# Kernel optimization log

Hardware: AMD Instinct MI355X
Metric: run time of the kernel (lower is better)

## Reference

```python
import jax, jax.numpy as jnp
import numpy as np

D = 512       # d_model
M = 64        # working memory_dim
SE = 32       # episodic slots
SS = 64       # semantic slots
H = 4         # episodic heads
B, L = 2, 1024
BOT = max(D // 4, 32)  # controller bottleneck = 128


def _layernorm(x, g, b, eps=1e-5):
    mu = jnp.mean(x, axis=-1, keepdims=True)
    var = jnp.var(x, axis=-1, keepdims=True)
    return (x - mu) * jax.lax.rsqrt(var + eps) * g + b


def setup_inputs() -> dict:
    key = jax.random.key(0)
    ks = jax.random.split(key, 24)
    r = lambda i, shape, s=0.02: jax.random.normal(ks[i], shape, dtype=jnp.float32) * s
    return {
        "x": jax.random.normal(ks[0], (B, L, D), dtype=jnp.float32),
        # WorkingMemory (weights stored as (in, out))
        "Wq": r(1, (D, M)), "Wk": r(2, (D, M)), "Wv": r(3, (D, D)),
        "Wf": r(4, (D, M)), "bf": jnp.zeros((M,), jnp.float32),
        "Wo": r(5, (D, D)),
        "ln_g": jnp.ones((D,), jnp.float32), "ln_b": jnp.zeros((D,), jnp.float32),
        # EpisodicMemory
        "eslots": r(6, (1, SE, D)),
        "Eq": r(7, (D, D)), "Ek": r(8, (D, D)), "Ev": r(9, (D, D)), "Eo": r(10, (D, D)),
        # SemanticMemory
        "know": r(11, (1, SS, D)),
        "Sin": r(12, (D, D)),
        "Sg_w": r(13, (D, D)), "Sg_b": jnp.zeros((D,), jnp.float32),
        "So": r(14, (D, D)),
        # MemoryController
        "C1w": r(15, (D, BOT)), "C1b": jnp.zeros((BOT,), jnp.float32),
        "C2w": r(16, (BOT, 3)), "C2b": jnp.zeros((3,), jnp.float32),
    }


def _forward(x, Wq, Wk, Wv, Wf, bf, Wo, ln_g, ln_b,
             eslots, Eq, Ek, Ev, Eo,
             know, Sin, Sg_w, Sg_b, So,
             C1w, C1b, C2w, C2b):
    b, l, d = x.shape
    # ---- WorkingMemory (parallel gated linear attention) ----
    scale = M ** -0.5
    q = (jax.nn.elu(x @ Wq) + 1.0) * scale          # (B,L,M)
    k = jax.nn.elu(x @ Wk) + 1.0                    # (B,L,M)
    v = x @ Wv                                      # (B,L,D)
    forget = jax.nn.sigmoid(x @ Wf + bf)            # (B,L,M)
    log_f_cum = jnp.clip(jnp.cumsum(jnp.log(jnp.clip(forget, 1e-6, None)), axis=1), -20.0, 20.0)
    exp_neg = jnp.exp(-log_f_cum)
    exp_pos = jnp.exp(log_f_cum)
    kv = k[..., :, None] * v[..., None, :]          # (B,L,M,D) outer product
    cum_kv = jnp.cumsum(exp_neg[..., None] * kv, axis=1)
    Mstate = exp_pos[..., None] * cum_kv            # (B,L,M,D)
    z = exp_pos * jnp.cumsum(exp_neg * k, axis=1)   # (B,L,M)
    num = jnp.einsum('blm,blmd->bld', q, Mstate)
    den = jnp.einsum('blm,blm->bl', q, z)[..., None] + 1e-6
    w_out = _layernorm(num / den, ln_g, ln_b) @ Wo  # (B,L,D)

    # ---- EpisodicMemory (cross-attn to learned slots) ----
    hd = D // H
    mem = jnp.broadcast_to(eslots, (b, SE, D))
    qh = (x @ Eq).reshape(b, l, H, hd)
    kh = (mem @ Ek).reshape(b, SE, H, hd)
    vh = (mem @ Ev).reshape(b, SE, H, hd)
    scores = jnp.einsum('blhe,bshe->bhls', qh, kh) / jnp.sqrt(jnp.float32(hd))
    attn = jax.nn.softmax(scores, axis=-1)
    e_out = jnp.einsum('bhls,bshe->blhe', attn, vh).reshape(b, l, D) @ Eo

    # ---- SemanticMemory (single-head attn to knowledge, gated residual) ----
    kb = jnp.broadcast_to(know, (b, SS, D))
    qs = x @ Sin                                    # (B,L,D)
    s_scores = jnp.einsum('bld,bsd->bls', qs, kb) / jnp.sqrt(jnp.float32(D))
    s_attn = jax.nn.softmax(s_scores, axis=-1)
    retrieved = jnp.einsum('bls,bsd->bld', s_attn, kb)
    gate = jax.nn.sigmoid(x @ Sg_w + Sg_b)
    s_out = (gate * retrieved + (1.0 - gate) * x) @ So

    # ---- Controller fusion ----
    wts = jax.nn.softmax(jax.nn.silu(x @ C1w + C1b) @ C2w + C2b, axis=-1)  # (B,L,3)
    fused = (wts[..., 0:1] * w_out + wts[..., 1:2] * e_out + wts[..., 2:3] * s_out)
    return fused


def reference(x, Wq, Wk, Wv, Wf, bf, Wo, ln_g, ln_b,
              eslots, Eq, Ek, Ev, Eo,
              know, Sin, Sg_w, Sg_b, So,
              C1w, C1b, C2w, C2b):
    return _forward(x, Wq, Wk, Wv, Wf, bf, Wo, ln_g, ln_b,
                    eslots, Eq, Ek, Ev, Eo,
                    know, Sin, Sg_w, Sg_b, So,
                    C1w, C1b, C2w, C2b)
```

## Files before the change

kernel.cpp:

```cpp
#include <hip/hip_runtime.h>
#include <cstdint>

typedef unsigned int uint;
typedef unsigned short ushort;
typedef __attribute__((ext_vector_type(8))) short bf16x8;
typedef __attribute__((ext_vector_type(4))) float f32x4;

__device__ __forceinline__ ushort f2b(float f) {
  union { float f; uint u; } v; v.f = f;
  uint u = v.u;
  uint r = (u + 0x7FFFu + ((u >> 16) & 1u)) >> 16;
  return (ushort)r;
}
__device__ __forceinline__ float b2f(ushort h) {
  union { uint u; float f; } v; v.u = ((uint)h) << 16; return v.f;
}

__global__ __launch_bounds__(256) void k_prepA(
    const float* __restrict__ know, const float* __restrict__ eslots,
    const float* __restrict__ Ek, const float* __restrict__ Ev, const float* __restrict__ Sin,
    ushort* __restrict__ Wcat, float* __restrict__ kh, float* __restrict__ vh)
{
  int bid = blockIdx.x;
  int tid = threadIdx.x;
  int lane = tid & 63, wv = tid >> 6;

  if (bid < 256) {
    int k = bid * 2 + (wv >> 1);
    int s0 = (wv & 1) * 32;
    const float* sp = Sin + (size_t)k * 512 + lane * 8;
    float4 s1 = *(const float4*)&sp[0];
    float4 s2 = *(const float4*)&sp[4];
    #pragma unroll 4
    for (int si = 0; si < 32; ++si) {
      int s = s0 + si;
      const float* kp = know + (size_t)s * 512 + lane * 8;
      float4 k1 = *(const float4*)&kp[0];
      float4 k2 = *(const float4*)&kp[4];
      float part = s1.x * k1.x + s1.y * k1.y + s1.z * k1.z + s1.w * k1.w
                 + s2.x * k2.x + s2.y * k2.y + s2.z * k2.z + s2.w * k2.w;
      #pragma unroll
      for (int o = 32; o; o >>= 1) part += __shfl_xor(part, o);
      if (lane == 0) Wcat[(640 + s) * 512 + k] = f2b(part * 0.04419417382415922f);
    }
    return;
  }
  {
    int t = (bid - 256) * 256 + tid;
    int isv = (t >= 16384);
    int o = t & 16383; int s = o >> 9, j = o & 511;
    const float* W = isv ? Ev : Ek;
    const float* es = eslots + (size_t)s * 512;
    float a0 = 0.f, a1 = 0.f, a2 = 0.f, a3 = 0.f;
    #pragma unroll 8
    for (int d = 0; d < 512; d += 4) {
      a0 += es[d + 0] * W[(size_t)(d + 0) * 512 + j];
      a1 += es[d + 1] * W[(size_t)(d + 1) * 512 + j];
      a2 += es[d + 2] * W[(size_t)(d + 2) * 512 + j];
      a3 += es[d + 3] * W[(size_t)(d + 3) * 512 + j];
    }
    float acc = (a0 + a1) + (a2 + a3);
    (isv ? vh : kh)[(size_t)s * 512 + j] = acc;
  }
}

__global__ __launch_bounds__(256) void k_prepB(
    const float* __restrict__ x, const float* __restrict__ Wv, const float* __restrict__ Sg,
    const float* __restrict__ C1w, const float* __restrict__ Wq, const float* __restrict__ Wk,
    const float* __restrict__ Wf, const float* __restrict__ Wo, const float* __restrict__ So,
    const float* __restrict__ Eq, const float* __restrict__ Eo, const float* __restrict__ know,
    const float* __restrict__ kh, const float* __restrict__ vh,
    ushort* __restrict__ X16, ushort* __restrict__ Wcat, ushort* __restrict__ Wfin,
    ushort* __restrict__ know16)
{
  __shared__ __align__(16) float pool[4160];
  int bid = blockIdx.x;
  int tid = threadIdx.x;
  int lane = tid & 63, wv = tid >> 6;

  if (bid < 256) {
    int gw = bid * 4 + wv;
    #pragma unroll
    for (int pp = 0; pp < 2; ++pp) {
      int pair = gw * 2 + pp;
      int k = pair >> 2, h = pair & 3;
      const float* ep = Eq + (size_t)k * 512 + h * 128 + lane * 2;
      float e0 = ep[0], e1 = ep[1];
      #pragma unroll 4
      for (int s = 0; s < 32; ++s) {
        const float* kp = kh + (size_t)s * 512 + h * 128 + lane * 2;
        float part = e0 * kp[0] + e1 * kp[1];
        #pragma unroll
        for (int o = 32; o; o >>= 1) part += __shfl_xor(part, o);
        if (lane == 0) Wcat[(512 + h * 32 + s) * 512 + k] = f2b(part * 0.08838834764831845f);
      }
    }
    return;
  }
  if (bid < 512) {
    int o = (bid - 256) * 256 + tid;
    int hs = o >> 9, j = o & 511;
    int h = hs >> 5, s = hs & 31;
    const float* vhp = vh + (size_t)s * 512 + h * 128;
    float acc = 0.f;
    #pragma unroll 16
    for (int e = 0; e < 128; ++e) acc += vhp[e] * Eo[(size_t)(h * 128 + e) * 512 + j];
    Wfin[(size_t)j * 1152 + 1024 + hs] = f2b(acc);
    return;
  }
  if (bid < 808) {
    #define Tm(a,b) pool[(a) * 65 + (b)]
    int tt = bid - 512;
    const float* src; ushort* dst; int sld, dld, Nt, drow, dcol;
    if (tt < 64)       {           src = Wv;  dst = Wcat; sld = 512; dld = 512;  Nt = 8; drow = 0;    dcol = 0;   }
    else if (tt < 128) { tt -= 64; src = Sg;  dst = Wcat; sld = 512; dld = 512;  Nt = 8; drow = 704;  dcol = 0;   }
    else if (tt < 144) { tt -= 128; src = C1w; dst = Wcat; sld = 128; dld = 512; Nt = 2; drow = 1216; dcol = 0;   }
    else if (tt < 152) { tt -= 144; src = Wq;  dst = Wcat; sld = 64;  dld = 512; Nt = 1; drow = 1344; dcol = 0;   }
    else if (tt < 160) { tt -= 152; src = Wk;  dst = Wcat; sld = 64;  dld = 512; Nt = 1; drow = 1408; dcol = 0;   }
    else if (tt < 168) { tt -= 160; src = Wf;  dst = Wcat; sld = 64;  dld = 512; Nt = 1; drow = 1472; dcol = 0;   }
    else if (tt < 232) { tt -= 168; src = Wo;  dst = Wfin; sld = 512; dld = 1152; Nt = 8; drow = 0;   dcol = 0;   }
    else               { tt -= 232; src = So;  dst = Wfin; sld = 512; dld = 1152; Nt = 8; drow = 0;   dcol = 512; }
    int tk = tt / Nt, tn = tt % Nt;
    int k0 = tk * 64, n0 = tn * 64;
    int r = tid >> 4, c = (tid & 15) * 4;
    #pragma unroll
    for (int p = 0; p < 4; ++p) {
      int kk = p * 16 + r;
      float4 v = *(const float4*)&src[(size_t)(k0 + kk) * sld + n0 + c];
      Tm(c + 0, kk) = v.x; Tm(c + 1, kk) = v.y; Tm(c + 2, kk) = v.z; Tm(c + 3, kk) = v.w;
    }
    __syncthreads();
    int n = tid >> 2, kc = (tid & 3) * 16;
    uint u[8];
    #pragma unroll
    for (int j = 0; j < 8; ++j) {
      ushort lo = f2b(Tm(n, kc + 2 * j));
      ushort hi = f2b(Tm(n, kc + 2 * j + 1));
      u[j] = (uint)lo | ((uint)hi << 16);
    }
    size_t off = (size_t)(drow + n0 + n) * dld + dcol + k0 + kc;
    uint4 o1; o1.x = u[0]; o1.y = u[1]; o1.z = u[2]; o1.w = u[3];
    uint4 o2; o2.x = u[4]; o2.y = u[5]; o2.z = u[6]; o2.w = u[7];
    *(uint4*)&dst[off] = o1;
    *(uint4*)&dst[off + 8] = o2;
    #undef Tm
    return;
  }
  if (bid < 936) {
    int base = (bid - 808) * 256 + tid;
    #pragma unroll
    for (int it = 0; it < 8; ++it) {
      int t = base + it * 32768;
      float4 xv = *(const float4*)&x[(size_t)t * 4];
      uint2 o;
      o.x = (uint)f2b(xv.x) | ((uint)f2b(xv.y) << 16);
      o.y = (uint)f2b(xv.z) | ((uint)f2b(xv.w) << 16);
      *(uint2*)&X16[(size_t)t * 4] = o;
    }
    return;
  }
  {
    int t = (bid - 936) * 256 + tid;
    #pragma unroll
    for (int j = 0; j < 2; ++j) {
      float4 v = *(const float4*)&know[(size_t)t * 8 + j * 4];
      uint2 o;
      o.x = (uint)f2b(v.x) | ((uint)f2b(v.y) << 16);
      o.y = (uint)f2b(v.z) | ((uint)f2b(v.w) << 16);
      *(uint2*)&know16[(size_t)t * 8 + j * 4] = o;
    }
  }
}

__global__ __launch_bounds__(256) void k_gemm1(
    const ushort* __restrict__ A, const ushort* __restrict__ Bw, float* __restrict__ C,
    const float* __restrict__ sgb, const float* __restrict__ c1b, const float* __restrict__ bfb)
{
  __shared__ __align__(16) ushort As[64 * 32];
  __shared__ __align__(16) ushort Bs[128 * 32];
  int tid = threadIdx.x;
  int lane = tid & 63, wv = tid >> 6;
  int wm = (wv & 1) * 32, wn = (wv >> 1) * 64;
  int lr = lane & 15, lk = lane >> 4;
  int m0 = blockIdx.y * 64, n0 = blockIdx.x * 128;
  f32x4 zero4 = {0.f, 0.f, 0.f, 0.f};
  f32x4 acc[2][4];
  #pragma unroll
  for (int a = 0; a < 2; ++a)
    #pragma unroll
    for (int b = 0; b < 4; ++b) acc[a][b] = zero4;
  for (int kt = 0; kt < 16; ++kt) {
    int k0 = kt * 32;
    {
      int p = tid, row = p >> 2, cc = p & 3;
      int cs = cc ^ ((row >> 1) & 3);
      *(uint4*)&As[p * 8] = *(const uint4*)&A[(size_t)(m0 + row) * 512 + k0 + cs * 8];
    }
    #pragma unroll
    for (int i = 0; i < 2; ++i) {
      int p = i * 256 + tid, row = p >> 2, cc = p & 3;
      int cs = cc ^ ((row >> 1) & 3);
      *(uint4*)&Bs[p * 8] = *(const uint4*)&Bw[(size_t)(n0 + row) * 512 + k0 + cs * 8];
    }
    __syncthreads();
    bf16x8 af[2], bfv[4];
    #pragma unroll
    for (int mi = 0; mi < 2; ++mi) {
      int row = wm + mi * 16 + lr;
      int cc = lk ^ ((row >> 1) & 3);
      af[mi] = *(bf16x8*)&As[row * 32 + cc * 8];
    }
    #pragma unroll
    for (int ni = 0; ni < 4; ++ni) {
      int row = wn + ni * 16 + lr;
      int cc = lk ^ ((row >> 1) & 3);
      bfv[ni] = *(bf16x8*)&Bs[row * 32 + cc * 8];
    }
    #pragma unroll
    for (int mi = 0; mi < 2; ++mi)
      #pragma unroll
      for (int ni = 0; ni < 4; ++ni)
        acc[mi][ni] = __builtin_amdgcn_mfma_f32_16x16x32_bf16(af[mi], bfv[ni], acc[mi][ni], 0, 0, 0);
    __syncthreads();
  }
  #pragma unroll
  for (int mi = 0; mi < 2; ++mi) {
    #pragma unroll
    for (int ni = 0; ni < 4; ++ni) {
      int col = n0 + wn + ni * 16 + lr;
      #pragma unroll
      for (int r = 0; r < 4; ++r) {
        int rowb = m0 + wm + mi * 16 + lk * 4 + r;
        float v = acc[mi][ni][r];
        if (col >= 704) {
          if (col < 1216) { v = 1.f / (1.f + __expf(-(v + sgb[col - 704]))); }
          else if (col < 1344) { float tt = v + c1b[col - 1216]; v = tt / (1.f + __expf(-tt)); }
          else if (col < 1408) { float e = (v > 0.f) ? v : (__expf(v) - 1.f); v = (e + 1.f) * 0.125f; }
          else if (col < 1472) { float e = (v > 0.f) ? v : (__expf(v) - 1.f); v = e + 1.f; }
          else { float logit = v + bfb[col - 1472];
                 float s = 1.f / (1.f + expf(-logit));
                 v = logf(fmaxf(s, 1e-6f)); }
        }
        C[(size_t)rowb * 1536 + col] = v;
      }
    }
  }
}

__global__ __launch_bounds__(256) void k_gemm2(
    const ushort* __restrict__ A, const ushort* __restrict__ Bw, float* __restrict__ C)
{
  __shared__ __align__(16) ushort As[64 * 32];
  __shared__ __align__(16) ushort Bs[64 * 32];
  int tid = threadIdx.x;
  int lane = tid & 63, wv = tid >> 6;
  int wm = (wv & 1) * 32, wn = (wv >> 1) * 32;
  int lr = lane & 15, lk = lane >> 4;
  int m0 = blockIdx.y * 64, n0 = blockIdx.x * 64;
  f32x4 zero4 = {0.f, 0.f, 0.f, 0.f};
  f32x4 acc[2][2];
  #pragma unroll
  for (int a = 0; a < 2; ++a)
    #pragma unroll
    for (int b = 0; b < 2; ++b) acc[a][b] = zero4;
  for (int kt = 0; kt < 36; ++kt) {
    int k0 = kt * 32;
    {
      int p = tid, row = p >> 2, cc = p & 3;
      int cs = cc ^ ((row >> 1) & 3);
      *(uint4*)&As[p * 8] = *(const uint4*)&A[(size_t)(m0 + row) * 1152 + k0 + cs * 8];
      *(uint4*)&Bs[p * 8] = *(const uint4*)&Bw[(size_t)(n0 + row) * 1152 + k0 + cs * 8];
    }
    __syncthreads();
    bf16x8 af[2], bfv[2];
    #pragma unroll
    for (int mi = 0; mi < 2; ++mi) {
      int row = wm + mi * 16 + lr;
      int cc = lk ^ ((row >> 1) & 3);
      af[mi] = *(bf16x8*)&As[row * 32 + cc * 8];
    }
    #pragma unroll
    for (int ni = 0; ni < 2; ++ni) {
      int row = wn + ni * 16 + lr;
      int cc = lk ^ ((row >> 1) & 3);
      bfv[ni] = *(bf16x8*)&Bs[row * 32 + cc * 8];
    }
    #pragma unroll
    for (int mi = 0; mi < 2; ++mi)
      #pragma unroll
      for (int ni = 0; ni < 2; ++ni)
        acc[mi][ni] = __builtin_amdgcn_mfma_f32_16x16x32_bf16(af[mi], bfv[ni], acc[mi][ni], 0, 0, 0);
    __syncthreads();
  }
  #pragma unroll
  for (int mi = 0; mi < 2; ++mi) {
    #pragma unroll
    for (int ni = 0; ni < 2; ++ni) {
      int col = n0 + wn + ni * 16 + lr;
      #pragma unroll
      for (int r = 0; r < 4; ++r) {
        int rowb = m0 + wm + mi * 16 + lk * 4 + r;
        C[(size_t)rowb * 512 + col] = acc[mi][ni][r];
      }
    }
  }
}

__global__ __launch_bounds__(256) void k_gate(
    const float* __restrict__ P,
    float* __restrict__ cn, float* __restrict__ qe, float* __restrict__ qz)
{
  __shared__ float wsumA[4];
  __shared__ float wsumB[4];
  int bid = blockIdx.x;
  int tid = threadIdx.x;
  int b = bid >> 6, m = bid & 63;
  int lane = tid & 63, wv = tid >> 6;
  size_t rbase = (size_t)b * 1024 + tid * 4;

  float v0 = P[(rbase + 0) * 1536 + 1472 + m];
  float v1 = P[(rbase + 1) * 1536 + 1472 + m];
  float v2 = P[(rbase + 2) * 1536 + 1472 + m];
  float v3 = P[(rbase + 3) * 1536 + 1472 + m];
  v1 += v0; v2 += v1; v3 += v2;
  float tsum = v3;
  float sc = tsum;
  #pragma unroll
  for (int o = 1; o < 64; o <<= 1) {
    float t = __shfl_up(sc, o, 64);
    if (lane >= o) sc += t;
  }
  if (lane == 63) wsumA[wv] = sc;
  __syncthreads();
  float excl = sc - tsum;
  #pragma unroll
  for (int w2 = 0; w2 < 3; ++w2) if (w2 < wv) excl += wsumA[w2];

  float vv[4] = {v0, v1, v2, v3};
  float cv[4], qv[4];
  #pragma unroll
  for (int i = 0; i < 4; ++i) {
    size_t r = rbase + i;
    float lf = fminf(fmaxf(excl + vv[i], -20.f), 20.f);
    float en = expf(-lf), ep = expf(lf);
    float kk = P[r * 1536 + 1408 + m];
    float qq = P[r * 1536 + 1344 + m];
    cv[i] = en * kk;
    qv[i] = qq * ep;
    cn[r * 64 + m] = cv[i];
    qe[r * 64 + m] = qv[i];
  }

  float c1 = cv[0], c2 = c1 + cv[1], c3 = c2 + cv[2], c4 = c3 + cv[3];
  float t2 = c4;
  float sc2 = t2;
  #pragma unroll
  for (int o = 1; o < 64; o <<= 1) {
    float t = __shfl_up(sc2, o, 64);
    if (lane >= o) sc2 += t;
  }
  if (lane == 63) wsumB[wv] = sc2;
  __syncthreads();
  float excl2 = sc2 - t2;
  #pragma unroll
  for (int w2 = 0; w2 < 3; ++w2) if (w2 < wv) excl2 += wsumB[w2];

  float pr[4] = {c1, c2, c3, c4};
  #pragma unroll
  for (int i = 0; i < 4; ++i) {
    size_t r = rbase + i;
    qz[r * 64 + m] = qv[i] * (excl2 + pr[i]);
  }
}

__global__ __launch_bounds__(256) void k_scanA(
    const float* __restrict__ cn, const float* __restrict__ P, float* __restrict__ Send)
{
  __shared__ __align__(16) float cnS[32 * 64];
  __shared__ __align__(16) float vS[16 * 64];
  int tid = threadIdx.x;
  int bid = blockIdx.x;
  int dt = bid & 7, c = (bid >> 3) & 31, b = bid >> 8;
  int rb0 = b * 1024 + c * 32;
  #pragma unroll
  for (int it = 0; it < 2; ++it) {
    int p = it * 256 + tid;
    int row = p >> 4, c4f = (p & 15) * 4;
    *(float4*)&cnS[row * 64 + c4f] = *(const float4*)&cn[(size_t)(rb0 + row) * 64 + c4f];
  }
  __syncthreads();
  int mg = tid >> 4, dl = tid & 15;
  float4 acc[4];
  #pragma unroll
  for (int i = 0; i < 4; ++i) acc[i] = make_float4(0.f, 0.f, 0.f, 0.f);
  for (int ig = 0; ig < 2; ++ig) {
    int rb = rb0 + ig * 16;
    int row = tid >> 4, c4f = (tid & 15) * 4;
    *(float4*)&vS[row * 64 + c4f] = *(const float4*)&P[(size_t)(rb + row) * 1536 + dt * 64 + c4f];
    __syncthreads();
    #pragma unroll 4
    for (int i = 0; i < 16; ++i) {
      float4 vv = *(float4*)&vS[i * 64 + dl * 4];
      float4 cm = *(float4*)&cnS[(ig * 16 + i) * 64 + mg * 4];
      acc[0].x += cm.x * vv.x; acc[0].y += cm.x * vv.y; acc[0].z += cm.x * vv.z; acc[0].w += cm.x * vv.w;
      acc[1].x += cm.y * vv.x; acc[1].y += cm.y * vv.y; acc[1].z += cm.y * vv.z; acc[1].w += cm.y * vv.w;
      acc[2].x += cm.z * vv.x; acc[2].y += cm.z * vv.y; acc[2].z += cm.z * vv.z; acc[2].w += cm.z * vv.w;
      acc[3].x += cm.w * vv.x; acc[3].y += cm.w * vv.y; acc[3].z += cm.w * vv.z; acc[3].w += cm.w * vv.w;
    }
    __syncthreads();
  }
  #pragma unroll
  for (int mi = 0; mi < 4; ++mi) {
    int m = mg * 4 + mi;
    *(float4*)&Send[(size_t)((b * 32 + c) * 64 + m) * 512 + dt * 64 + dl * 4] = acc[mi];
  }
}

__global__ __launch_bounds__(256) void k_scanB(const float* __restrict__ Send, float* __restrict__ carry)
{
  int t = blockIdx.x * 256 + threadIdx.x;
  int d = t & 511, m = (t >> 9) & 63, b = t >> 15;
  float run = 0.f;
  #pragma unroll 8
  for (int c = 0; c < 32; ++c) {
    size_t idx = (size_t)((b * 32 + c) * 64 + m) * 512 + d;
    carry[idx] = run;
    run += Send[idx];
  }
}

__global__ __launch_bounds__(256) void k_scanC(
    const float* __restrict__ cn, const float* __restrict__ qe, const float* __restrict__ P,
    const float* __restrict__ carry, float* __restrict__ num)
{
  __shared__ __align__(16) float cnS[32 * 64];
  __shared__ __align__(16) float qeS[32 * 64];
  __shared__ __align__(16) float vS[16 * 64];
  int tid = threadIdx.x;
  int bid = blockIdx.x;
  int dt = bid & 7, c = (bid >> 3) & 31, b = bid >> 8;
  int rb0 = b * 1024 + c * 32;
  #pragma unroll
  for (int it = 0; it < 2; ++it) {
    int p = it * 256 + tid;
    int row = p >> 4, c4f = (p & 15) * 4;
    *(float4*)&cnS[row * 64 + c4f] = *(const float4*)&cn[(size_t)(rb0 + row) * 64 + c4f];
    *(float4*)&qeS[row * 64 + c4f] = *(const float4*)&qe[(size_t)(rb0 + row) * 64 + c4f];
  }
  int mg = tid & 3, dl = tid >> 2;
  int d = dt * 64 + dl;
  float S[16];
  #pragma unroll
  for (int mi = 0; mi < 16; ++mi)
    S[mi] = carry[(size_t)((b * 32 + c) * 64 + mg * 16 + mi) * 512 + d];
  __syncthreads();
  for (int ig = 0; ig < 2; ++ig) {
    int rb = rb0 + ig * 16;
    int row = tid >> 4, c4f = (tid & 15) * 4;
    *(float4*)&vS[row * 64 + c4f] = *(const float4*)&P[(size_t)(rb + row) * 1536 + dt * 64 + c4f];
    __syncthreads();
    for (int i = 0; i < 16; ++i) {
      int ii = ig * 16 + i;
      float vv = vS[i * 64 + dl];
      float p = 0.f;
      #pragma unroll
      for (int j = 0; j < 4; ++j) {
        float4 c4 = *(float4*)&cnS[ii * 64 + mg * 16 + j * 4];
        float4 q4 = *(float4*)&qeS[ii * 64 + mg * 16 + j * 4];
        S[j * 4 + 0] += c4.x * vv; p += q4.x * S[j * 4 + 0];
        S[j * 4 + 1] += c4.y * vv; p += q4.y * S[j * 4 + 1];
        S[j * 4 + 2] += c4.z * vv; p += q4.z * S[j * 4 + 2];
        S[j * 4 + 3] += c4.w * vv; p += q4.w * S[j * 4 + 3];
      }
      p += __shfl_xor(p, 1);
      p += __shfl_xor(p, 2);
      if (mg == 0) num[(size_t)(rb0 + ii) * 512 + d] = p;
    }
    __syncthreads();
  }
}

__global__ __launch_bounds__(256) void k_post(
    const float* __restrict__ P, const float* __restrict__ x,
    const float* __restrict__ num, const float* __restrict__ qz,
    const ushort* __restrict__ know16, const float* __restrict__ lng,
    const float* __restrict__ lnb, const float* __restrict__ C2w,
    const float* __restrict__ C2b, ushort* __restrict__ Afin)
{
  __shared__ __align__(16) ushort kbuf[32 * 512];
  __shared__ float attnL[4][64];
  __shared__ float w2L[4];
  int tid = threadIdx.x;
  int w = tid >> 6, lane = tid & 63;
  int r0 = blockIdx.x * 4;
  int r = r0 + w;
  size_t pr = (size_t)r * 1536;

  float h0 = P[pr + 1216 + lane], h1 = P[pr + 1280 + lane];
  float a0 = h0 * C2w[lane * 3 + 0] + h1 * C2w[(64 + lane) * 3 + 0];
  float a1 = h0 * C2w[lane * 3 + 1] + h1 * C2w[(64 + lane) * 3 + 1];
  float a2 = h0 * C2w[lane * 3 + 2] + h1 * C2w[(64 + lane) * 3 + 2];
  #pragma unroll
  for (int o = 32; o; o >>= 1) {
    a0 += __shfl_xor(a0, o); a1 += __shfl_xor(a1, o); a2 += __shfl_xor(a2, o);
  }
  a0 += C2b[0]; a1 += C2b[1]; a2 += C2b[2];
  float mxc = fmaxf(a0, fmaxf(a1, a2));
  float e0 = expf(a0 - mxc), e1 = expf(a1 - mxc), e2c = expf(a2 - mxc);
  float inv = 1.f / (e0 + e1 + e2c);
  float w0 = e0 * inv, w1 = e1 * inv, w2 = e2c * inv;
  if (lane == 0) w2L[w] = w2;

  {
    float den = qz[(size_t)r * 64 + lane];
    #pragma unroll
    for (int o = 32; o; o >>= 1) den += __shfl_xor(den, o);
    den += 1e-6f;
    float y[8];
    float4 n0 = *(const float4*)&num[(size_t)r * 512 + lane * 8];
    float4 n1 = *(const float4*)&num[(size_t)r * 512 + lane * 8 + 4];
    y[0] = n0.x / den; y[1] = n0.y / den; y[2] = n0.z / den; y[3] = n0.w / den;
    y[4] = n1.x / den; y[5] = n1.y / den; y[6] = n1.z / den; y[7] = n1.w / den;
    float s1 = 0.f, s2 = 0.f;
    #pragma unroll
    for (int i = 0; i < 8; ++i) { s1 += y[i]; s2 += y[i] * y[i]; }
    #pragma unroll
    for (int o = 32; o; o >>= 1) { s1 += __shfl_xor(s1, o); s2 += __shfl_xor(s2, o); }
    float mu = s1 * (1.f / 512.f);
    float var = s2 * (1.f / 512.f) - mu * mu;
    float rs = rsqrtf(var + 1e-5f);
    uint4 outv;
    uint pk[4];
    #pragma unroll
    for (int p2 = 0; p2 < 4; ++p2) {
      float o0 = (y[2 * p2] - mu) * rs * lng[lane * 8 + 2 * p2] + lnb[lane * 8 + 2 * p2];
      float o1 = (y[2 * p2 + 1] - mu) * rs * lng[lane * 8 + 2 * p2 + 1] + lnb[lane * 8 + 2 * p2 + 1];
      pk[p2] = (uint)f2b(o0 * w0) | ((uint)f2b(o1 * w0) << 16);
    }
    outv.x = pk[0]; outv.y = pk[1]; outv.z = pk[2]; outv.w = pk[3];
    *(uint4*)&Afin[(size_t)r * 1152 + lane * 8] = outv;
  }

  {
    int h = lane >> 4, ei = (lane & 15) * 2;
    float v0 = P[pr + 512 + h * 32 + ei], v1 = P[pr + 512 + h * 32 + ei + 1];
    float mxe = fmaxf(v0, v1);
    #pragma unroll
    for (int o = 1; o < 16; o <<= 1) mxe = fmaxf(mxe, __shfl_xor(mxe, o));
    float ee0 = __expf(v0 - mxe), ee1 = __expf(v1 - mxe);
    float ss = ee0 + ee1;
    #pragma unroll
    for (int o = 1; o < 16; o <<= 1) ss += __shfl_xor(ss, o);
    float sc1 = w1 / ss;
    uint pkv = (uint)f2b(ee0 * sc1) | ((uint)f2b(ee1 * sc1) << 16);
    *(uint*)&Afin[(size_t)r * 1152 + 1024 + h * 32 + ei] = pkv;
  }

  {
    float lv = P[pr + 640 + lane];
    float mx = lv;
    #pragma unroll
    for (int o = 32; o; o >>= 1) mx = fmaxf(mx, __shfl_xor(mx, o));
    float e = __expf(lv - mx);
    float sum = e;
    #pragma unroll
    for (int o = 32; o; o >>= 1) sum += __shfl_xor(sum, o);
    attnL[w][lane] = e / sum;
  }
  __syncthreads();

  int dd = tid * 2;
  float acc[4][2];
  #pragma unroll
  for (int i = 0; i < 4; ++i) { acc[i][0] = 0.f; acc[i][1] = 0.f; }
  for (int hs = 0; hs < 2; ++hs) {
    #pragma unroll
    for (int i = 0; i < 8; ++i) {
      int idx = i * 256 + tid;
      *(uint4*)&kbuf[idx * 8] = *(const uint4*)&know16[(size_t)hs * 16384 + idx * 8];
    }
    __syncthreads();
    for (int s = 0; s < 32; ++s) {
      uint uu = *(uint*)&kbuf[s * 512 + dd];
      float k0 = b2f((ushort)(uu & 0xffff));
      float k1 = b2f((ushort)(uu >> 16));
      #pragma unroll
      for (int row = 0; row < 4; ++row) {
        float a = attnL[row][hs * 32 + s];
        acc[row][0] += a * k0;
        acc[row][1] += a * k1;
      }
    }
    __syncthreads();
  }
  #pragma unroll
  for (int row = 0; row < 4; ++row) {
    int rr = r0 + row;
    float g0 = P[(size_t)rr * 1536 + 704 + dd];
    float g1 = P[(size_t)rr * 1536 + 704 + dd + 1];
    float x0 = x[(size_t)rr * 512 + dd], x1 = x[(size_t)rr * 512 + dd + 1];
    float w2v = w2L[row];
    float m0 = g0 * acc[row][0] + (1.f - g0) * x0;
    float m1 = g1 * acc[row][1] + (1.f - g1) * x1;
    uint pkv = (uint)f2b(w2v * m0) | ((uint)f2b(w2v * m1) << 16);
    *(uint*)&Afin[(size_t)rr * 1152 + 512 + dd] = pkv;
  }
}

extern "C" void kernel_launch(void* const* d_in, const int* in_sizes, int n_in,
                              void* d_out, int out_size, void* d_ws, size_t ws_size,
                              hipStream_t stream)
{
  const float* x     = (const float*)d_in[0];
  const float* Wq    = (const float*)d_in[1];
  const float* Wk    = (const float*)d_in[2];
  const float* Wv    = (const float*)d_in[3];
  const float* Wf    = (const float*)d_in[4];
  const float* bfb   = (const float*)d_in[5];
  const float* Wo    = (const float*)d_in[6];
  const float* ln_g  = (const float*)d_in[7];
  const float* ln_b  = (const float*)d_in[8];
  const float* eslots= (const float*)d_in[9];
  const float* Eq    = (const float*)d_in[10];
  const float* Ek    = (const float*)d_in[11];
  const float* Ev    = (const float*)d_in[12];
  const float* Eo    = (const float*)d_in[13];
  const float* know  = (const float*)d_in[14];
  const float* Sin   = (const float*)d_in[15];
  const float* Sg_w  = (const float*)d_in[16];
  const float* Sg_b  = (const float*)d_in[17];
  const float* So    = (const float*)d_in[18];
  const float* C1w   = (const float*)d_in[19];
  const float* C1b   = (const float*)d_in[20];
  const float* C2w   = (const float*)d_in[21];
  const float* C2b   = (const float*)d_in[22];

  char* ws = (char*)d_ws;
  ushort* X16    = (ushort*)(ws + 0);
  ushort* Wcat   = (ushort*)(ws + 2097152);
  ushort* Wfin   = (ushort*)(ws + 3670016);
  ushort* know16 = (ushort*)(ws + 4849664);
  float*  kh     = (float*)(ws + 4915200);
  float*  vh     = (float*)(ws + 4980736);
  float*  P      = (float*)(ws + 5046272);
  float*  cn     = (float*)(ws + 18153472);
  float*  qe     = (float*)(ws + 18677760);
  float*  qz     = (float*)(ws + 19202048);
  float*  Send   = (float*)(ws + 19726336);
  float*  carry  = (float*)(ws + 28114944);
  float*  num    = (float*)(ws + 36503552);
  ushort* Afin   = (ushort*)(ws + 40697856);

  k_prepA<<<dim3(384), dim3(256), 0, stream>>>(know, eslots, Ek, Ev, Sin, Wcat, kh, vh);
  k_prepB<<<dim3(952), dim3(256), 0, stream>>>(x, Wv, Sg_w, C1w, Wq, Wk, Wf, Wo, So,
                                               Eq, Eo, know, kh, vh,
                                               X16, Wcat, Wfin, know16);
  k_gemm1<<<dim3(12, 32), dim3(256), 0, stream>>>(X16, Wcat, P, Sg_b, C1b, bfb);
  k_gate<<<dim3(128), dim3(256), 0, stream>>>(P, cn, qe, qz);
  k_scanA<<<dim3(512), dim3(256), 0, stream>>>(cn, P, Send);
  k_scanB<<<dim3(256), dim3(256), 0, stream>>>(Send, carry);
  k_scanC<<<dim3(512), dim3(256), 0, stream>>>(cn, qe, P, carry, num);
  k_post<<<dim3(512), dim3(256), 0, stream>>>(P, x, num, qz, know16, ln_g, ln_b, C2w, C2b, Afin);
  k_gemm2<<<dim3(8, 32), dim3(256), 0, stream>>>(Afin, Wfin, (float*)d_out);
}
```

Measured before the change: 131.2 us.

## Fuse gate cumsum into gemm1 epilogue and scan kernels, drop k_gate

Removes the separate k_gate kernel. The gemm1 epilogue for the forget-gate tile now writes partial log-forget sums over groups of 16 rows into s16. The scan kernels rebuild the running prefix from those partials and apply exp(-lf) and exp(lf) to k and q directly from P. The normaliser sum is folded into scanC as a cumulative z, so k_post only reads a scalar per row. This saves one launch and the cn, qe and qz round trips, at the cost of redundant prefix work in each scan block and serial loops over earlier chunks.

```diff
diff --git a/kernel.cpp b/kernel.cpp
--- a/kernel.cpp
+++ b/kernel.cpp
@@ -174,10 +174,13 @@
 
 __global__ __launch_bounds__(256) void k_gemm1(
     const ushort* __restrict__ A, const ushort* __restrict__ Bw, float* __restrict__ C,
-    const float* __restrict__ sgb, const float* __restrict__ c1b, const float* __restrict__ bfb)
-{
-  __shared__ __align__(16) ushort As[64 * 32];
-  __shared__ __align__(16) ushort Bs[128 * 32];
+    const float* __restrict__ sgb, const float* __restrict__ c1b, const float* __restrict__ bfb,
+    float* __restrict__ s16)
+{
+  __shared__ __align__(16) char poolraw[24832];
+  ushort* As = (ushort*)poolraw;
+  ushort* Bs = As + 2048;
+  float* sf = (float*)poolraw;
   int tid = threadIdx.x;
   int lane = tid & 63, wv = tid >> 6;
   int wm = (wv & 1) * 32, wn = (wv >> 1) * 64;
@@ -223,6 +226,7 @@
         acc[mi][ni] = __builtin_amdgcn_mfma_f32_16x16x32_bf16(af[mi], bfv[ni], acc[mi][ni], 0, 0, 0);
     __syncthreads();
   }
+  int isFblk = (n0 == 1408);
   #pragma unroll
   for (int mi = 0; mi < 2; ++mi) {
     #pragma unroll
@@ -239,11 +243,20 @@
           else if (col < 1472) { float e = (v > 0.f) ? v : (__expf(v) - 1.f); v = e + 1.f; }
           else { float logit = v + bfb[col - 1472];
                  float s = 1.f / (1.f + expf(-logit));
-                 v = logf(fmaxf(s, 1e-6f)); }
+                 v = logf(fmaxf(s, 1e-6f));
+                 if (isFblk) sf[(wm + mi * 16 + lk * 4 + r) * 65 + (col - 1472)] = v; }
         }
         C[(size_t)rowb * 1536 + col] = v;
       }
     }
+  }
+  if (isFblk) {
+    __syncthreads();
+    int g = tid >> 6, m = tid & 63;
+    float s = 0.f;
+    #pragma unroll
+    for (int i = 0; i < 16; ++i) s += sf[(g * 16 + i) * 65 + m];
+    s16[(size_t)(blockIdx.y * 4 + g) * 64 + m] = s;
   }
 }
 
@@ -306,78 +319,15 @@
   }
 }
 
-__global__ __launch_bounds__(256) void k_gate(
-    const float* __restrict__ P,
-    float* __restrict__ cn, float* __restrict__ qe, float* __restrict__ qz)
-{
-  __shared__ float wsumA[4];
-  __shared__ float wsumB[4];
-  int bid = blockIdx.x;
-  int tid = threadIdx.x;
-  int b = bid >> 6, m = bid & 63;
-  int lane = tid & 63, wv = tid >> 6;
-  size_t rbase = (size_t)b * 1024 + tid * 4;
-
-  float v0 = P[(rbase + 0) * 1536 + 1472 + m];
-  float v1 = P[(rbase + 1) * 1536 + 1472 + m];
-  float v2 = P[(rbase + 2) * 1536 + 1472 + m];
-  float v3 = P[(rbase + 3) * 1536 + 1472 + m];
-  v1 += v0; v2 += v1; v3 += v2;
-  float tsum = v3;
-  float sc = tsum;
-  #pragma unroll
-  for (int o = 1; o < 64; o <<= 1) {
-    float t = __shfl_up(sc, o, 64);
-    if (lane >= o) sc += t;
-  }
-  if (lane == 63) wsumA[wv] = sc;
-  __syncthreads();
-  float excl = sc - tsum;
-  #pragma unroll
-  for (int w2 = 0; w2 < 3; ++w2) if (w2 < wv) excl += wsumA[w2];
-
-  float vv[4] = {v0, v1, v2, v3};
-  float cv[4], qv[4];
-  #pragma unroll
-  for (int i = 0; i < 4; ++i) {
-    size_t r = rbase + i;
-    float lf = fminf(fmaxf(excl + vv[i], -20.f), 20.f);
-    float en = expf(-lf), ep = expf(lf);
-    float kk = P[r * 1536 + 1408 + m];
-    float qq = P[r * 1536 + 1344 + m];
-    cv[i] = en * kk;
-    qv[i] = qq * ep;
-    cn[r * 64 + m] = cv[i];
-    qe[r * 64 + m] = qv[i];
-  }
-
-  float c1 = cv[0], c2 = c1 + cv[1], c3 = c2 + cv[2], c4 = c3 + cv[3];
-  float t2 = c4;
-  float sc2 = t2;
-  #pragma unroll
-  for (int o = 1; o < 64; o <<= 1) {
-    float t = __shfl_up(sc2, o, 64);
-    if (lane >= o) sc2 += t;
-  }
-  if (lane == 63) wsumB[wv] = sc2;
-  __syncthreads();
-  float excl2 = sc2 - t2;
-  #pragma unroll
-  for (int w2 = 0; w2 < 3; ++w2) if (w2 < wv) excl2 += wsumB[w2];
-
-  float pr[4] = {c1, c2, c3, c4};
-  #pragma unroll
-  for (int i = 0; i < 4; ++i) {
-    size_t r = rbase + i;
-    qz[r * 64 + m] = qv[i] * (excl2 + pr[i]);
-  }
-}
-
 __global__ __launch_bounds__(256) void k_scanA(
-    const float* __restrict__ cn, const float* __restrict__ P, float* __restrict__ Send)
-{
-  __shared__ __align__(16) float cnS[32 * 64];
+    const float* __restrict__ P, const float* __restrict__ s16,
+    float* __restrict__ Send, float* __restrict__ zSend)
+{
+  __shared__ __align__(16) float lfS[32 * 64];
+  __shared__ __align__(16) float kS[32 * 64];
   __shared__ __align__(16) float vS[16 * 64];
+  __shared__ float bpP[4][64];
+  __shared__ float zsP[2][64];
   int tid = threadIdx.x;
   int bid = blockIdx.x;
   int dt = bid & 7, c = (bid >> 3) & 31, b = bid >> 8;
@@ -386,9 +336,35 @@
   for (int it = 0; it < 2; ++it) {
     int p = it * 256 + tid;
     int row = p >> 4, c4f = (p & 15) * 4;
-    *(float4*)&cnS[row * 64 + c4f] = *(const float4*)&cn[(size_t)(rb0 + row) * 64 + c4f];
+    *(float4*)&lfS[row * 64 + c4f] = *(const float4*)&P[(size_t)(rb0 + row) * 1536 + 1472 + c4f];
+    *(float4*)&kS[row * 64 + c4f] = *(const float4*)&P[(size_t)(rb0 + row) * 1536 + 1408 + c4f];
+  }
+  {
+    int m = tid & 63, gq = tid >> 6;
+    float part = 0.f;
+    for (int g = gq; g < c * 2; g += 4) part += s16[(size_t)(b * 64 + g) * 64 + m];
+    bpP[gq][m] = part;
   }
   __syncthreads();
+  if (tid < 128) {
+    int mq = tid & 63, q = tid >> 6;
+    float run = bpP[0][mq] + bpP[1][mq] + bpP[2][mq] + bpP[3][mq];
+    if (q == 1) run += s16[(size_t)(b * 64 + c * 2) * 64 + mq];
+    float zs = 0.f;
+    #pragma unroll
+    for (int i = 0; i < 16; ++i) {
+      int row = q * 16 + i;
+      run += lfS[row * 64 + mq];
+      float lf = fminf(fmaxf(run, -20.f), 20.f);
+      float cv = __expf(-lf) * kS[row * 64 + mq];
+      kS[row * 64 + mq] = cv;
+      zs += cv;
+    }
+    zsP[q][mq] = zs;
+  }
+  __syncthreads();
+  if (dt == 0 && tid < 64)
+    zSend[(size_t)(b * 32 + c) * 64 + tid] = zsP[0][tid] + zsP[1][tid];
   int mg = tid >> 4, dl = tid & 15;
   float4 acc[4];
   #pragma unroll
@@ -401,7 +377,7 @@
     #pragma unroll 4
     for (int i = 0; i < 16; ++i) {
       float4 vv = *(float4*)&vS[i * 64 + dl * 4];
-      float4 cm = *(float4*)&cnS[(ig * 16 + i) * 64 + mg * 4];
+      float4 cm = *(float4*)&kS[(ig * 16 + i) * 64 + mg * 4];
       acc[0].x += cm.x * vv.x; acc[0].y += cm.x * vv.y; acc[0].z += cm.x * vv.z; acc[0].w += cm.x * vv.w;
       acc[1].x += cm.y * vv.x; acc[1].y += cm.y * vv.y; acc[1].z += cm.y * vv.z; acc[1].w += cm.y * vv.w;
       acc[2].x += cm.z * vv.x; acc[2].y += cm.z * vv.y; acc[2].z += cm.z * vv.z; acc[2].w += cm.z * vv.w;
@@ -430,12 +406,15 @@
 }
 
 __global__ __launch_bounds__(256) void k_scanC(
-    const float* __restrict__ cn, const float* __restrict__ qe, const float* __restrict__ P,
-    const float* __restrict__ carry, float* __restrict__ num)
-{
+    const float* __restrict__ P, const float* __restrict__ s16,
+    const float* __restrict__ carry, const float* __restrict__ zSend,
+    float* __restrict__ num, float* __restrict__ den)
+{
+  __shared__ __align__(16) float lfS[32 * 64];
   __shared__ __align__(16) float cnS[32 * 64];
-  __shared__ __align__(16) float qeS[32 * 64];
+  __shared__ __align__(16) float qS[32 * 64];
   __shared__ __align__(16) float vS[16 * 64];
+  __shared__ float bpP[4][64];
   int tid = threadIdx.x;
   int bid = blockIdx.x;
   int dt = bid & 7, c = (bid >> 3) & 31, b = bid >> 8;
@@ -444,16 +423,48 @@
   for (int it = 0; it < 2; ++it) {
     int p = it * 256 + tid;
     int row = p >> 4, c4f = (p & 15) * 4;
-    *(float4*)&cnS[row * 64 + c4f] = *(const float4*)&cn[(size_t)(rb0 + row) * 64 + c4f];
-    *(float4*)&qeS[row * 64 + c4f] = *(const float4*)&qe[(size_t)(rb0 + row) * 64 + c4f];
-  }
+    *(float4*)&lfS[row * 64 + c4f] = *(const float4*)&P[(size_t)(rb0 + row) * 1536 + 1472 + c4f];
+    *(float4*)&cnS[row * 64 + c4f] = *(const float4*)&P[(size_t)(rb0 + row) * 1536 + 1408 + c4f];
+    *(float4*)&qS[row * 64 + c4f] = *(const float4*)&P[(size_t)(rb0 + row) * 1536 + 1344 + c4f];
+  }
+  {
+    int m = tid & 63, gq = tid >> 6;
+    float part = 0.f;
+    for (int g = gq; g < c * 2; g += 4) part += s16[(size_t)(b * 64 + g) * 64 + m];
+    bpP[gq][m] = part;
+  }
+  __syncthreads();
+  if (tid < 128) {
+    int mq = tid & 63, q = tid >> 6;
+    float run = bpP[0][mq] + bpP[1][mq] + bpP[2][mq] + bpP[3][mq];
+    if (q == 1) run += s16[(size_t)(b * 64 + c * 2) * 64 + mq];
+    #pragma unroll
+    for (int i = 0; i < 16; ++i) {
+      int row = q * 16 + i;
+      run += lfS[row * 64 + mq];
+      float lf = fminf(fmaxf(run, -20.f), 20.f);
+      float en = __expf(-lf), ep = __expf(lf);
+      cnS[row * 64 + mq] = en * cnS[row * 64 + mq];
+      qS[row * 64 + mq] = qS[row * 64 + mq] * ep;
+    }
+  }
+  __syncthreads();
   int mg = tid & 3, dl = tid >> 2;
   int d = dt * 64 + dl;
   float S[16];
-  #pragma unroll
-  for (int mi = 0; mi < 16; ++mi)
+  float z16[16];
+  #pragma unroll
+  for (int mi = 0; mi < 16; ++mi) {
     S[mi] = carry[(size_t)((b * 32 + c) * 64 + mg * 16 + mi) * 512 + d];
-  __syncthreads();
+    z16[mi] = 0.f;
+  }
+  if (dt == 0) {
+    for (int j = 0; j < c; ++j) {
+      size_t zb = (size_t)(b * 32 + j) * 64 + mg * 16;
+      #pragma unroll
+      for (int mi = 0; mi < 16; ++mi) z16[mi] += zSend[zb + mi];
+    }
+  }
   for (int ig = 0; ig < 2; ++ig) {
     int rb = rb0 + ig * 16;
     int row = tid >> 4, c4f = (tid & 15) * 4;
@@ -463,18 +474,30 @@
       int ii = ig * 16 + i;
       float vv = vS[i * 64 + dl];
       float p = 0.f;
+      float dp = 0.f;
       #pragma unroll
       for (int j = 0; j < 4; ++j) {
         float4 c4 = *(float4*)&cnS[ii * 64 + mg * 16 + j * 4];
-        float4 q4 = *(float4*)&qeS[ii * 64 + mg * 16 + j * 4];
+        float4 q4 = *(float4*)&qS[ii * 64 + mg * 16 + j * 4];
         S[j * 4 + 0] += c4.x * vv; p += q4.x * S[j * 4 + 0];
         S[j * 4 + 1] += c4.y * vv; p += q4.y * S[j * 4 + 1];
         S[j * 4 + 2] += c4.z * vv; p += q4.z * S[j * 4 + 2];
         S[j * 4 + 3] += c4.w * vv; p += q4.w * S[j * 4 + 3];
+        if (dt == 0) {
+          z16[j * 4 + 0] += c4.x; dp += q4.x * z16[j * 4 + 0];
+          z16[j * 4 + 1] += c4.y; dp += q4.y * z16[j * 4 + 1];
+          z16[j * 4 + 2] += c4.z; dp += q4.z * z16[j * 4 + 2];
+          z16[j * 4 + 3] += c4.w; dp += q4.w * z16[j * 4 + 3];
+        }
       }
       p += __shfl_xor(p, 1);
       p += __shfl_xor(p, 2);
       if (mg == 0) num[(size_t)(rb0 + ii) * 512 + d] = p;
+      if (dt == 0) {
+        dp += __shfl_xor(dp, 1);
+        dp += __shfl_xor(dp, 2);
+        if (mg == 0 && dl == 0) den[rb0 + ii] = dp;
+      }
     }
     __syncthreads();
   }
@@ -482,7 +505,7 @@
 
 __global__ __launch_bounds__(256) void k_post(
     const float* __restrict__ P, const float* __restrict__ x,
-    const float* __restrict__ num, const float* __restrict__ qz,
+    const float* __restrict__ num, const float* __restrict__ denB,
     const ushort* __restrict__ know16, const float* __restrict__ lng,
     const float* __restrict__ lnb, const float* __restrict__ C2w,
     const float* __restrict__ C2b, ushort* __restrict__ Afin)
@@ -512,15 +535,12 @@
   if (lane == 0) w2L[w] = w2;
 
   {
-    float den = qz[(size_t)r * 64 + lane];
-    #pragma unroll
-    for (int o = 32; o; o >>= 1) den += __shfl_xor(den, o);
-    den += 1e-6f;
+    float dv = denB[r] + 1e-6f;
     float y[8];
     float4 n0 = *(const float4*)&num[(size_t)r * 512 + lane * 8];
     float4 n1 = *(const float4*)&num[(size_t)r * 512 + lane * 8 + 4];
-    y[0] = n0.x / den; y[1] = n0.y / den; y[2] = n0.z / den; y[3] = n0.w / den;
-    y[4] = n1.x / den; y[5] = n1.y / den; y[6] = n1.z / den; y[7] = n1.w / den;
+    y[0] = n0.x / dv; y[1] = n0.y / dv; y[2] = n0.z / dv; y[3] = n0.w / dv;
+    y[4] = n1.x / dv; y[5] = n1.y / dv; y[6] = n1.z / dv; y[7] = n1.w / dv;
     float s1 = 0.f, s2 = 0.f;
     #pragma unroll
     for (int i = 0; i < 8; ++i) { s1 += y[i]; s2 += y[i] * y[i]; }
@@ -643,9 +663,9 @@
   float*  kh     = (float*)(ws + 4915200);
   float*  vh     = (float*)(ws + 4980736);
   float*  P      = (float*)(ws + 5046272);
-  float*  cn     = (float*)(ws + 18153472);
-  float*  qe     = (float*)(ws + 18677760);
-  float*  qz     = (float*)(ws + 19202048);
+  float*  s16    = (float*)(ws + 18153472);
+  float*  zSend  = (float*)(ws + 18677760);
+  float*  den    = (float*)(ws + 19202048);
   float*  Send   = (float*)(ws + 19726336);
   float*  carry  = (float*)(ws + 28114944);
   float*  num    = (float*)(ws + 36503552);
@@ -655,11 +675,10 @@
   k_prepB<<<dim3(952), dim3(256), 0, stream>>>(x, Wv, Sg_w, C1w, Wq, Wk, Wf, Wo, So,
                                                Eq, Eo, know, kh, vh,
                                                X16, Wcat, Wfin, know16);
-  k_gemm1<<<dim3(12, 32), dim3(256), 0, stream>>>(X16, Wcat, P, Sg_b, C1b, bfb);
-  k_gate<<<dim3(128), dim3(256), 0, stream>>>(P, cn, qe, qz);
-  k_scanA<<<dim3(512), dim3(256), 0, stream>>>(cn, P, Send);
+  k_gemm1<<<dim3(12, 32), dim3(256), 0, stream>>>(X16, Wcat, P, Sg_b, C1b, bfb, s16);
+  k_scanA<<<dim3(512), dim3(256), 0, stream>>>(P, s16, Send, zSend);
   k_scanB<<<dim3(256), dim3(256), 0, stream>>>(Send, carry);
-  k_scanC<<<dim3(512), dim3(256), 0, stream>>>(cn, qe, P, carry, num);
-  k_post<<<dim3(512), dim3(256), 0, stream>>>(P, x, num, qz, know16, ln_g, ln_b, C2w, C2b, Afin);
+  k_scanC<<<dim3(512), dim3(256), 0, stream>>>(P, s16, carry, zSend, num, den);
+  k_post<<<dim3(512), dim3(256), 0, stream>>>(P, x, num, den, know16, ln_g, ln_b, C2w, C2b, Afin);
   k_gemm2<<<dim3(8, 32), dim3(256), 0, stream>>>(Afin, Wfin, (float*)d_out);
 }
```

Result: slower. 151.5 us (+15.5%).
